# Kernel optimization log

Measured on AMD Instinct MI355X. Metric: run time of the kernel, lower is better.

Reference implementation:

```python
import jax, jax.numpy as jnp
import numpy as np

D_MODEL = 2048
N_Q_HEADS = 32
N_KV_HEADS = 8
D_HEAD = 64
D_MLP = 8192
NORM_EPS = 1e-5
INIT_RANGE = 0.02
IGNORE = -100000.0
B, S = 2, 2048


def setup_inputs() -> dict:
    key = jax.random.key(0)
    ks = jax.random.split(key, 8)
    return {
        "resid_pre": jax.random.normal(ks[0], (B, S, D_MODEL), dtype=jnp.float32),
        "W_Q": jax.random.normal(ks[1], (N_Q_HEADS, D_MODEL, D_HEAD), dtype=jnp.float32) * INIT_RANGE,
        "W_K": jax.random.normal(ks[2], (N_KV_HEADS, D_MODEL, D_HEAD), dtype=jnp.float32) * INIT_RANGE,
        "W_V": jax.random.normal(ks[3], (N_KV_HEADS, D_MODEL, D_HEAD), dtype=jnp.float32) * INIT_RANGE,
        "W_O": jax.random.normal(ks[4], (N_KV_HEADS, D_HEAD, D_MODEL), dtype=jnp.float32) * INIT_RANGE,
        "g1": jnp.ones((D_MODEL,), jnp.float32),
        "b1": jnp.zeros((D_MODEL,), jnp.float32),
        "g2": jnp.ones((D_MODEL,), jnp.float32),
        "b2": jnp.zeros((D_MODEL,), jnp.float32),
        "W_in": jax.random.normal(ks[5], (D_MODEL, D_MLP), dtype=jnp.float32) * INIT_RANGE,
        "b_in": jnp.zeros((D_MLP,), jnp.float32),
        "W_out": jax.random.normal(ks[6], (D_MLP, D_MODEL), dtype=jnp.float32) * INIT_RANGE,
        "b_out": jnp.zeros((D_MODEL,), jnp.float32),
    }


def rmsnorm(x, g, b):
    # torch.var (unbiased=False) is mean-centered variance, but x itself is
    # divided (not centered) -- faithful to the source.
    mu = jnp.mean(x, axis=-1, keepdims=True)
    var = jnp.mean(jnp.square(x - mu), axis=-1, keepdims=True)
    std = jnp.sqrt(var + NORM_EPS)
    return (x / std) * g + b


def attention(x, W_Q, W_K, W_V, W_O):
    b, s, _ = x.shape
    q = jnp.einsum('bpd,hde->bphe', x, W_Q)            # [b, s, n_q, d_head]
    k = jnp.einsum('bpd,hde->bphe', x, W_K)            # [b, s, n_kv, d_head]
    v = jnp.einsum('bpd,hde->bphe', x, W_V)            # [b, s, n_kv, d_head]
    g_size = N_Q_HEADS // N_KV_HEADS
    # rearrange '(n_kv g) d' with n_kv outer, group inner
    q = q.reshape(b, s, N_KV_HEADS, g_size, D_HEAD)
    # source einsum sums over the group dim (g not in output) -- faithful
    scores = jnp.einsum('bqkgd,bskd->bkqs', q, k) / jnp.sqrt(jnp.float32(D_HEAD))
    mask = jnp.triu(jnp.ones((s, s), dtype=bool), k=1)
    scores = jnp.where(mask, jnp.float32(IGNORE), scores)
    pattern = jax.nn.softmax(scores, axis=-1)          # [b, n_kv, q, s]
    z = jnp.einsum('bskd,bkqs->bqkd', v, pattern)      # [b, q, n_kv, d_head]
    return jnp.einsum('bqkd,kde->bqe', z, W_O)


def ffn(x, W_in, b_in, W_out, b_out):
    pre = jnp.einsum('bpd,dm->bpm', x, W_in) + b_in
    post = jax.nn.relu(pre)
    return jnp.einsum('bpm,md->bpd', post, W_out) + b_out


def reference(resid_pre, W_Q, W_K, W_V, W_O, g1, b1, g2, b2, W_in, b_in, W_out, b_out):
    resid_mid = attention(rmsnorm(resid_pre, g1, b1), W_Q, W_K, W_V, W_O) + resid_pre
    resid_post = ffn(rmsnorm(resid_mid, g2, b2), W_in, b_in, W_out, b_out) + resid_mid
    return resid_post
```

## Files before the change

kernel.cpp:

```cpp
#include <hip/hip_runtime.h>
#include <hip/hip_bf16.h>


using bf16 = __hip_bfloat16;
typedef __bf16 bf16x8_t __attribute__((ext_vector_type(8)));
typedef float  f32x4_t  __attribute__((ext_vector_type(4)));

#define D_MODEL 2048
#define SEQ     2048
#define NB      2
#define NTOK    4096
#define NKV     8
#define DHEAD   64
#define DMLP    8192
#define NQKV    1536

__device__ inline void storev(float* p, float v) { *p = v; }
__device__ inline void storev(bf16* p, float v)  { *p = __float2bfloat16(v); }

__device__ inline bf16 h_from_b(__bf16 x) {
    union { __bf16 b; bf16 h; } u;
    u.b = x;
    return u.h;
}

__global__ __launch_bounds__(256) void transpose_f32_bf16_kernel(
    const float* __restrict__ in, bf16* __restrict__ out, int K, int N)
{
    __shared__ float tile[32][33];
    const int n0 = blockIdx.x * 32, k0 = blockIdx.y * 32;
    const int tx = threadIdx.x & 31, ty = threadIdx.x >> 5;
    #pragma unroll
    for (int i = 0; i < 32; i += 8)
        tile[ty + i][tx] = in[(size_t)(k0 + ty + i) * N + n0 + tx];
    __syncthreads();
    #pragma unroll
    for (int i = 0; i < 32; i += 8)
        out[(size_t)(n0 + ty + i) * K + k0 + tx] = __float2bfloat16(tile[tx][ty + i]);
}

__global__ __launch_bounds__(256) void head_transpose_kernel(
    const float* __restrict__ in, bf16* __restrict__ out, int ngroup)
{
    __shared__ float tile[32][65];
    const int kv = blockIdx.y;
    const int k0 = blockIdx.x * 32;
    const int t  = threadIdx.x;
    const int e  = t & 63, kk = t >> 6;
    #pragma unroll
    for (int i = 0; i < 32; i += 4) {
        float s = 0.f;
        for (int g = 0; g < ngroup; ++g)
            s += in[((size_t)(kv * ngroup + g) * 2048 + k0 + kk + i) * 64 + e];
        tile[kk + i][e] = s;
    }
    __syncthreads();
    const int k = t & 31, ee = t >> 5;
    #pragma unroll
    for (int i = 0; i < 64; i += 8)
        out[(size_t)(kv * 64 + ee + i) * 2048 + k0 + k] = __float2bfloat16(tile[k][ee + i]);
}

__global__ __launch_bounds__(256) void rmsnorm_kernel(
    const float* __restrict__ x, const float* __restrict__ g,
    const float* __restrict__ b, bf16* __restrict__ out)
{
    const int row = blockIdx.x;
    const int t = threadIdx.x;
    const float* xr = x + (size_t)row * D_MODEL;
    float4 a0 = *reinterpret_cast<const float4*>(xr + t * 8);
    float4 a1 = *reinterpret_cast<const float4*>(xr + t * 8 + 4);
    float v[8] = {a0.x, a0.y, a0.z, a0.w, a1.x, a1.y, a1.z, a1.w};
    float sum = 0.f, sumsq = 0.f;
    #pragma unroll
    for (int j = 0; j < 8; ++j) { sum += v[j]; sumsq += v[j] * v[j]; }
    #pragma unroll
    for (int o = 1; o < 64; o <<= 1) {
        sum   += __shfl_xor(sum, o);
        sumsq += __shfl_xor(sumsq, o);
    }
    __shared__ float rs[4], rq[4];
    if ((t & 63) == 0) { rs[t >> 6] = sum; rq[t >> 6] = sumsq; }
    __syncthreads();
    sum   = rs[0] + rs[1] + rs[2] + rs[3];
    sumsq = rq[0] + rq[1] + rq[2] + rq[3];
    const float mu  = sum * (1.f / D_MODEL);
    const float var = sumsq * (1.f / D_MODEL) - mu * mu;
    const float rstd = 1.f / sqrtf(var + 1e-5f);
    const int c = t * 8;
    float4 g0 = *reinterpret_cast<const float4*>(g + c);
    float4 g1 = *reinterpret_cast<const float4*>(g + c + 4);
    float4 b0 = *reinterpret_cast<const float4*>(b + c);
    float4 b1 = *reinterpret_cast<const float4*>(b + c + 4);
    float gg[8] = {g0.x, g0.y, g0.z, g0.w, g1.x, g1.y, g1.z, g1.w};
    float bb[8] = {b0.x, b0.y, b0.z, b0.w, b1.x, b1.y, b1.z, b1.w};
    bf16* op = out + (size_t)row * D_MODEL + c;
    #pragma unroll
    for (int j = 0; j < 8; ++j) op[j] = __float2bfloat16(v[j] * rstd * gg[j] + bb[j]);
}

template<int BM, int BN, typename TC, bool BIAS, bool RELU, bool RESID>
__global__ __launch_bounds__(512, 2) void gemm_pipe_kernel(
    const bf16* __restrict__ A, const bf16* __restrict__ Bt,
    TC* __restrict__ C, const float* __restrict__ bias,
    const float* __restrict__ resid, int M, int N, int K, int nbx)
{
    constexpr int BK   = 64;
    constexpr int MREP = BM / 32;
    constexpr int NREP = BN / 64;
    constexpr int AI   = (BM * BK) / 4096;
    constexpr int BI   = (BN * BK) / 4096;
    constexpr int LD   = AI + BI;

    __shared__ __align__(16) bf16 As[2][BM * BK];
    __shared__ __align__(16) bf16 Bs[2][BN * BK];

    const int nwg = gridDim.x;
    const int swz = (blockIdx.x & 7) * (nwg >> 3) + (blockIdx.x >> 3);
    const int nby = nwg / nbx;
    const int by  = swz % nby;
    const int bx  = swz / nby;
    const int row0 = by * BM, col0 = bx * BN;

    const int t  = threadIdx.x;
    const int w  = t >> 6, ln = t & 63;
    const int wm = w >> 2, wn = w & 3;
    const int lr = ln & 15, hi = ln >> 4;

    const int srow = w * 8 + (ln >> 3);
    const int skx  = ((ln & 7) ^ (ln >> 3)) * 8;

    f32x4_t acc[MREP][NREP];
    #pragma unroll
    for (int m = 0; m < MREP; ++m)
        #pragma unroll
        for (int n = 0; n < NREP; ++n) acc[m][n] = (f32x4_t){0.f, 0.f, 0.f, 0.f};

    const int NT = K / BK;

    {
        const bf16* ga = A  + (size_t)(row0 + srow) * K + skx;
        const bf16* gb = Bt + (size_t)(col0 + srow) * K + skx;
        #pragma unroll
        for (int i = 0; i < AI; ++i)
            __builtin_amdgcn_global_load_lds(
                (const __attribute__((address_space(1))) void*)(ga + (size_t)i * 64 * K),
                (__attribute__((address_space(3))) void*)(&As[0][i * 4096 + w * 512]), 16, 0, 0);
        #pragma unroll
        for (int i = 0; i < BI; ++i)
            __builtin_amdgcn_global_load_lds(
                (const __attribute__((address_space(1))) void*)(gb + (size_t)i * 64 * K),
                (__attribute__((address_space(3))) void*)(&Bs[0][i * 4096 + w * 512]), 16, 0, 0);
    }

    for (int tt = 0; tt < NT; ++tt) {
        const int c = tt & 1;
        asm volatile("s_waitcnt lgkmcnt(0)" ::: "memory");
        __builtin_amdgcn_sched_barrier(0);
        __builtin_amdgcn_s_barrier();
        __builtin_amdgcn_sched_barrier(0);
        if (tt + 1 < NT) {
            const int d = c ^ 1;
            const int kt = (tt + 1) * BK;
            const bf16* ga = A  + (size_t)(row0 + srow) * K + kt + skx;
            const bf16* gb = Bt + (size_t)(col0 + srow) * K + kt + skx;
            #pragma unroll
            for (int i = 0; i < AI; ++i)
                __builtin_amdgcn_global_load_lds(
                    (const __attribute__((address_space(1))) void*)(ga + (size_t)i * 64 * K),
                    (__attribute__((address_space(3))) void*)(&As[d][i * 4096 + w * 512]), 16, 0, 0);
            #pragma unroll
            for (int i = 0; i < BI; ++i)
                __builtin_amdgcn_global_load_lds(
                    (const __attribute__((address_space(1))) void*)(gb + (size_t)i * 64 * K),
                    (__attribute__((address_space(3))) void*)(&Bs[d][i * 4096 + w * 512]), 16, 0, 0);
            __builtin_amdgcn_sched_barrier(0);
            if constexpr (LD == 8)      asm volatile("s_waitcnt vmcnt(8)" ::: "memory");
            else if constexpr (LD == 6) asm volatile("s_waitcnt vmcnt(6)" ::: "memory");
            else                        asm volatile("s_waitcnt vmcnt(4)" ::: "memory");
        } else {
            asm volatile("s_waitcnt vmcnt(0)" ::: "memory");
        }
        __builtin_amdgcn_sched_barrier(0);
        __builtin_amdgcn_s_barrier();
        __builtin_amdgcn_sched_barrier(0);

        #pragma unroll
        for (int kk = 0; kk < 2; ++kk) {
            bf16x8_t af[MREP], bfr[NREP];
            #pragma unroll
            for (int m = 0; m < MREP; ++m) {
                const int row = wm * (BM / 2) + m * 16 + lr;
                af[m] = *reinterpret_cast<const bf16x8_t*>(
                    &As[c][row * 64 + ((kk * 32 + hi * 8) ^ ((row & 7) << 3))]);
            }
            #pragma unroll
            for (int n = 0; n < NREP; ++n) {
                const int col = wn * (BN / 4) + n * 16 + lr;
                bfr[n] = *reinterpret_cast<const bf16x8_t*>(
                    &Bs[c][col * 64 + ((kk * 32 + hi * 8) ^ ((col & 7) << 3))]);
            }
            #pragma unroll
            for (int m = 0; m < MREP; ++m)
                #pragma unroll
                for (int n = 0; n < NREP; ++n)
                    acc[m][n] = __builtin_amdgcn_mfma_f32_16x16x32_bf16(af[m], bfr[n], acc[m][n], 0, 0, 0);
        }
    }

    #pragma unroll
    for (int m = 0; m < MREP; ++m) {
        #pragma unroll
        for (int n = 0; n < NREP; ++n) {
            const int cgl = col0 + wn * (BN / 4) + n * 16 + lr;
            #pragma unroll
            for (int j = 0; j < 4; ++j) {
                const int r = row0 + wm * (BM / 2) + m * 16 + hi * 4 + j;
                float v = acc[m][n][j];
                if constexpr (BIAS)  v += bias[cgl];
                if constexpr (RELU)  v = fmaxf(v, 0.f);
                if constexpr (RESID) v += resid[(size_t)r * N + cgl];
                storev(&C[(size_t)r * N + cgl], v);
            }
        }
    }
}

template<typename TC, bool BIAS, bool RELU, bool RESID>
__global__ __launch_bounds__(512, 2) void gemm_8ph_kernel(
    const bf16* __restrict__ A, const bf16* __restrict__ Bt,
    TC* __restrict__ C, const float* __restrict__ bias,
    const float* __restrict__ resid, int M, int N, int K, int nbx)
{
    __shared__ __align__(16) bf16 As[2][256 * 64];
    __shared__ __align__(16) bf16 Bs[2][256 * 64];

    const int nwg = gridDim.x;
    const int swz = (blockIdx.x & 7) * (nwg >> 3) + (blockIdx.x >> 3);
    const int nby = nwg / nbx;
    const int by  = swz % nby;
    const int bx  = swz / nby;
    const int row0 = by * 256, col0 = bx * 256;

    const int t  = threadIdx.x;
    const int w  = t >> 6, ln = t & 63;
    const int wm = w >> 2, wn = w & 3;
    const int lr = ln & 15, hi = ln >> 4;
    const int rx = (lr & 7) << 3;

    const int srow = w * 8 + (ln >> 3);
    const int skx  = ((ln & 7) ^ (ln >> 3)) * 8;

#define STAGE_A8(u, dbuf, kt)                                                   \
    __builtin_amdgcn_global_load_lds(                                           \
        (const __attribute__((address_space(1))) void*)(A + (size_t)(row0 + (u) * 64 + srow) * K + (kt) + skx), \
        (__attribute__((address_space(3))) void*)(&As[dbuf][(u) * 4096 + w * 512]), 16, 0, 0)
#define STAGE_B8(u, dbuf, kt)                                                   \
    __builtin_amdgcn_global_load_lds(                                           \
        (const __attribute__((address_space(1))) void*)(Bt + (size_t)(col0 + (u) * 64 + srow) * K + (kt) + skx), \
        (__attribute__((address_space(3))) void*)(&Bs[dbuf][(u) * 4096 + w * 512]), 16, 0, 0)
#define PH_BAR                                                                  \
    __builtin_amdgcn_sched_barrier(0);                                          \
    __builtin_amdgcn_s_barrier();                                               \
    __builtin_amdgcn_sched_barrier(0)
#define LGKM0                                                                   \
    asm volatile("s_waitcnt lgkmcnt(0)" ::: "memory");                          \
    __builtin_amdgcn_sched_barrier(0)

    f32x4_t acc[8][4];
    #pragma unroll
    for (int m = 0; m < 8; ++m)
        #pragma unroll
        for (int n = 0; n < 4; ++n) acc[m][n] = (f32x4_t){0.f, 0.f, 0.f, 0.f};

    bf16x8_t af[4][2];
    bf16x8_t bfr[4][2];

    const int NT = K / 64;

    STAGE_A8(0, 0, 0); STAGE_A8(2, 0, 0);
    STAGE_B8(0, 0, 0); STAGE_B8(1, 0, 0); STAGE_B8(2, 0, 0); STAGE_B8(3, 0, 0);
    STAGE_A8(1, 0, 0); STAGE_A8(3, 0, 0);
    asm volatile("s_waitcnt vmcnt(2)" ::: "memory");
    PH_BAR;

    for (int tt = 0; tt < NT; ++tt) {
        const int c  = tt & 1, d = c ^ 1;
        const int kn = (tt + 1) * 64;
        const bool pf = (tt + 1 < NT);

        #pragma unroll
        for (int mq = 0; mq < 4; ++mq) {
            const int row = wm * 128 + mq * 16 + lr;
            #pragma unroll
            for (int kk = 0; kk < 2; ++kk)
                af[mq][kk] = *reinterpret_cast<const bf16x8_t*>(
                    &As[c][row * 64 + ((kk * 32 + hi * 8) ^ rx)]);
        }
        #pragma unroll
        for (int n = 0; n < 2; ++n) {
            const int col = wn * 64 + n * 16 + lr;
            #pragma unroll
            for (int kk = 0; kk < 2; ++kk)
                bfr[n][kk] = *reinterpret_cast<const bf16x8_t*>(
                    &Bs[c][col * 64 + ((kk * 32 + hi * 8) ^ rx)]);
        }
        if (pf) { STAGE_A8(0, d, kn); STAGE_A8(2, d, kn); }
        PH_BAR;
        LGKM0;
        __builtin_amdgcn_s_setprio(1);
        #pragma unroll
        for (int mq = 0; mq < 4; ++mq)
            #pragma unroll
            for (int n = 0; n < 2; ++n)
                #pragma unroll
                for (int kk = 0; kk < 2; ++kk)
                    acc[mq][n] = __builtin_amdgcn_mfma_f32_16x16x32_bf16(af[mq][kk], bfr[n][kk], acc[mq][n], 0, 0, 0);
        __builtin_amdgcn_s_setprio(0);
        PH_BAR;

        #pragma unroll
        for (int n = 2; n < 4; ++n) {
            const int col = wn * 64 + n * 16 + lr;
            #pragma unroll
            for (int kk = 0; kk < 2; ++kk)
                bfr[n][kk] = *reinterpret_cast<const bf16x8_t*>(
                    &Bs[c][col * 64 + ((kk * 32 + hi * 8) ^ rx)]);
        }
        if (pf) { STAGE_B8(0, d, kn); STAGE_B8(1, d, kn); }
        __builtin_amdgcn_sched_barrier(0);
        if (pf) { asm volatile("s_waitcnt vmcnt(4)" ::: "memory"); }
        else    { asm volatile("s_waitcnt vmcnt(0)" ::: "memory"); }
        PH_BAR;
        LGKM0;
        __builtin_amdgcn_s_setprio(1);
        #pragma unroll
        for (int mq = 0; mq < 4; ++mq)
            #pragma unroll
            for (int n = 2; n < 4; ++n)
                #pragma unroll
                for (int kk = 0; kk < 2; ++kk)
                    acc[mq][n] = __builtin_amdgcn_mfma_f32_16x16x32_bf16(af[mq][kk], bfr[n][kk], acc[mq][n], 0, 0, 0);
        __builtin_amdgcn_s_setprio(0);
        PH_BAR;

        #pragma unroll
        for (int mq = 0; mq < 4; ++mq) {
            const int row = wm * 128 + 64 + mq * 16 + lr;
            #pragma unroll
            for (int kk = 0; kk < 2; ++kk)
                af[mq][kk] = *reinterpret_cast<const bf16x8_t*>(
                    &As[c][row * 64 + ((kk * 32 + hi * 8) ^ rx)]);
        }
        if (pf) { STAGE_B8(2, d, kn); STAGE_B8(3, d, kn); }
        PH_BAR;
        LGKM0;
        __builtin_amdgcn_s_setprio(1);
        #pragma unroll
        for (int mq = 0; mq < 4; ++mq)
            #pragma unroll
            for (int n = 2; n < 4; ++n)
                #pragma unroll
                for (int kk = 0; kk < 2; ++kk)
                    acc[4 + mq][n] = __builtin_amdgcn_mfma_f32_16x16x32_bf16(af[mq][kk], bfr[n][kk], acc[4 + mq][n], 0, 0, 0);
        __builtin_amdgcn_s_setprio(0);
        PH_BAR;

        if (pf) {
            STAGE_A8(1, d, kn); STAGE_A8(3, d, kn);
            __builtin_amdgcn_sched_barrier(0);
            asm volatile("s_waitcnt vmcnt(2)" ::: "memory");
        }
        PH_BAR;
        __builtin_amdgcn_s_setprio(1);
        #pragma unroll
        for (int mq = 0; mq < 4; ++mq)
            #pragma unroll
            for (int n = 0; n < 2; ++n)
                #pragma unroll
                for (int kk = 0; kk < 2; ++kk)
                    acc[4 + mq][n] = __builtin_amdgcn_mfma_f32_16x16x32_bf16(af[mq][kk], bfr[n][kk], acc[4 + mq][n], 0, 0, 0);
        __builtin_amdgcn_s_setprio(0);
        PH_BAR;
    }

    #pragma unroll
    for (int m = 0; m < 8; ++m) {
        #pragma unroll
        for (int n = 0; n < 4; ++n) {
            const int cgl = col0 + wn * 64 + n * 16 + lr;
            #pragma unroll
            for (int j = 0; j < 4; ++j) {
                const int r = row0 + wm * 128 + m * 16 + hi * 4 + j;
                float v = acc[m][n][j];
                if constexpr (BIAS)  v += bias[cgl];
                if constexpr (RELU)  v = fmaxf(v, 0.f);
                if constexpr (RESID) v += resid[(size_t)r * N + cgl];
                storev(&C[(size_t)r * N + cgl], v);
            }
        }
    }
#undef STAGE_A8
#undef STAGE_B8
#undef PH_BAR
#undef LGKM0
}

#define KVBLK 64
#define LP    72

__global__ __launch_bounds__(256) void mfma_attn_kernel(
    const bf16* __restrict__ qkv, bf16* __restrict__ z)
{
    const int a  = blockIdx.x;
    const int kv = blockIdx.y;
    const int b  = blockIdx.z;
    const int b2 = 31 - a;
    const int t  = threadIdx.x;
    const int w  = t >> 6;
    const int ln = t & 63;
    const int lr = ln & 15;
    const int hi = ln >> 4;
    const int lk = hi * 8;

    __shared__ __align__(16) bf16 Ks[KVBLK * LP];
    __shared__ __align__(16) bf16 Vt[DHEAD * LP];
    __shared__ __align__(16) bf16 Ps[64 * LP];

    bf16x8_t qfA[2], qfB[2];
    #pragma unroll
    for (int sb = 0; sb < 2; ++sb) {
        const int qrow = (sb ? b2 : a) * 64 + w * 16 + lr;
        const bf16* qp = qkv + (size_t)(b * SEQ + qrow) * NQKV + kv * 64;
        #pragma unroll
        for (int kk = 0; kk < 2; ++kk) {
            bf16x8_t v = *reinterpret_cast<const bf16x8_t*>(qp + kk * 32 + lk);
            if (sb) qfB[kk] = v; else qfA[kk] = v;
        }
    }

    f32x4_t accA[4], accB[4];
    #pragma unroll
    for (int n = 0; n < 4; ++n) {
        accA[n] = (f32x4_t){0.f, 0.f, 0.f, 0.f};
        accB[n] = (f32x4_t){0.f, 0.f, 0.f, 0.f};
    }
    float mA[4] = {-1e30f, -1e30f, -1e30f, -1e30f}, lA[4] = {0.f, 0.f, 0.f, 0.f};
    float mB[4] = {-1e30f, -1e30f, -1e30f, -1e30f}, lB[4] = {0.f, 0.f, 0.f, 0.f};

    const int qcdA = a  * 64 + w * 16 + hi * 4;
    const int qcdB = 31 * 64 - a * 64 + w * 16 + hi * 4;

    auto process = [&](const bf16x8_t* qf, f32x4_t* acc_o, float* m_st,
                       float* l_st, int qcd, int k0g, bool diag) {
        f32x4_t s[4];
        #pragma unroll
        for (int n = 0; n < 4; ++n) s[n] = (f32x4_t){0.f, 0.f, 0.f, 0.f};
        #pragma unroll
        for (int kk = 0; kk < 2; ++kk) {
            #pragma unroll
            for (int n = 0; n < 4; ++n) {
                bf16x8_t kf = *reinterpret_cast<const bf16x8_t*>(&Ks[(n * 16 + lr) * LP + kk * 32 + lk]);
                s[n] = __builtin_amdgcn_mfma_f32_16x16x32_bf16(qf[kk], kf, s[n], 0, 0, 0);
            }
        }
        #pragma unroll
        for (int n = 0; n < 4; ++n) {
            const int colg = k0g + n * 16 + lr;
            #pragma unroll
            for (int j = 0; j < 4; ++j) {
                float val = s[n][j] * 0.125f;
                if (diag && colg > qcd + j) val = -1e30f;
                s[n][j] = val;
            }
        }
        float alpha[4], mnew[4];
        #pragma unroll
        for (int j = 0; j < 4; ++j) {
            float mx = fmaxf(fmaxf(s[0][j], s[1][j]), fmaxf(s[2][j], s[3][j]));
            mx = fmaxf(mx, __shfl_xor(mx, 1));
            mx = fmaxf(mx, __shfl_xor(mx, 2));
            mx = fmaxf(mx, __shfl_xor(mx, 4));
            mx = fmaxf(mx, __shfl_xor(mx, 8));
            mnew[j]  = fmaxf(m_st[j], mx);
            alpha[j] = __expf(m_st[j] - mnew[j]);
            m_st[j]  = mnew[j];
        }
        float psum[4] = {0.f, 0.f, 0.f, 0.f};
        #pragma unroll
        for (int n = 0; n < 4; ++n) {
            #pragma unroll
            for (int j = 0; j < 4; ++j) {
                float p = __expf(s[n][j] - mnew[j]);
                psum[j] += p;
                Ps[(w * 16 + hi * 4 + j) * LP + n * 16 + lr] = __float2bfloat16(p);
            }
        }
        #pragma unroll
        for (int j = 0; j < 4; ++j) {
            float ps = psum[j];
            ps += __shfl_xor(ps, 1);
            ps += __shfl_xor(ps, 2);
            ps += __shfl_xor(ps, 4);
            ps += __shfl_xor(ps, 8);
            l_st[j] = l_st[j] * alpha[j] + ps;
        }
        #pragma unroll
        for (int n = 0; n < 4; ++n)
            #pragma unroll
            for (int j = 0; j < 4; ++j)
                acc_o[n][j] *= alpha[j];
        #pragma unroll
        for (int kk = 0; kk < 2; ++kk) {
            bf16x8_t pa = *reinterpret_cast<const bf16x8_t*>(&Ps[(w * 16 + lr) * LP + kk * 32 + lk]);
            #pragma unroll
            for (int n = 0; n < 4; ++n) {
                bf16x8_t vf = *reinterpret_cast<const bf16x8_t*>(&Vt[(n * 16 + lr) * LP + kk * 32 + lk]);
                acc_o[n] = __builtin_amdgcn_mfma_f32_16x16x32_bf16(pa, vf, acc_o[n], 0, 0, 0);
            }
        }
    };

    for (int kt = 0; kt <= b2; ++kt) {
        const int k0g = kt * KVBLK;
        __syncthreads();
        {
            const int r   = t >> 2;
            const int c16 = (t & 3) * 16;
            const bf16* kb = qkv + (size_t)(b * SEQ + k0g + r) * NQKV + 512 + kv * 64 + c16;
            *reinterpret_cast<bf16x8_t*>(&Ks[r * LP + c16])     = *reinterpret_cast<const bf16x8_t*>(kb);
            *reinterpret_cast<bf16x8_t*>(&Ks[r * LP + c16 + 8]) = *reinterpret_cast<const bf16x8_t*>(kb + 8);
        }
        {
            const int dv = w * 16;
            const bf16* vb = qkv + (size_t)(b * SEQ + k0g + ln) * NQKV + 1024 + kv * 64 + dv;
            bf16x8_t v0 = *reinterpret_cast<const bf16x8_t*>(vb);
            bf16x8_t v1 = *reinterpret_cast<const bf16x8_t*>(vb + 8);
            #pragma unroll
            for (int i = 0; i < 8; ++i) {
                Vt[(dv + i)     * LP + ln] = h_from_b(v0[i]);
                Vt[(dv + 8 + i) * LP + ln] = h_from_b(v1[i]);
            }
        }
        __syncthreads();

        if (kt <= a) process(qfA, accA, mA, lA, qcdA, k0g, kt == a);
        process(qfB, accB, mB, lB, qcdB, k0g, kt == b2);
    }

    #pragma unroll
    for (int j = 0; j < 4; ++j) {
        const float invA = 1.f / lA[j];
        bf16* zpA = z + (size_t)(b * SEQ + qcdA + j) * (NKV * DHEAD) + kv * 64;
        const float invB = 1.f / lB[j];
        bf16* zpB = z + (size_t)(b * SEQ + qcdB + j) * (NKV * DHEAD) + kv * 64;
        #pragma unroll
        for (int n = 0; n < 4; ++n) {
            zpA[n * 16 + lr] = __float2bfloat16(accA[n][j] * invA);
            zpB[n * 16 + lr] = __float2bfloat16(accB[n][j] * invB);
        }
    }
}

extern "C" void kernel_launch(void* const* d_in, const int* in_sizes, int n_in,
                              void* d_out, int out_size, void* d_ws, size_t ws_size,
                              hipStream_t stream)
{
    const float* resid_pre = (const float*)d_in[0];
    const float* W_Q   = (const float*)d_in[1];
    const float* W_K   = (const float*)d_in[2];
    const float* W_V   = (const float*)d_in[3];
    const float* W_O   = (const float*)d_in[4];
    const float* g1    = (const float*)d_in[5];
    const float* b1    = (const float*)d_in[6];
    const float* g2    = (const float*)d_in[7];
    const float* b2    = (const float*)d_in[8];
    const float* W_in  = (const float*)d_in[9];
    const float* b_in  = (const float*)d_in[10];
    const float* W_out = (const float*)d_in[11];
    const float* b_out = (const float*)d_in[12];
    float* out = (float*)d_out;

    char* ws = (char*)d_ws;
    const size_t OFF_WBIG  = 0;
    const size_t OFF_WOT   = OFF_WBIG + (size_t)DMLP * D_MODEL * 2;
    const size_t OFF_X1    = OFF_WOT  + (size_t)D_MODEL * 512 * 2;
    const size_t OFF_RMID  = OFF_X1   + (size_t)NTOK * D_MODEL * 2;
    const size_t OFF_POST  = OFF_RMID + (size_t)NTOK * D_MODEL * 4;
    const size_t OFF_WQKVT = OFF_POST;
    const size_t OFF_QKV   = OFF_WQKVT + (size_t)NQKV * D_MODEL * 2;
    const size_t OFF_Z     = OFF_QKV   + (size_t)NTOK * NQKV * 2;

    bf16*  winT   = (bf16*) (ws + OFF_WBIG);
    bf16*  woutT  = (bf16*) (ws + OFF_WBIG);
    bf16*  woT    = (bf16*) (ws + OFF_WOT);
    bf16*  x1     = (bf16*) (ws + OFF_X1);
    float* rmid   = (float*)(ws + OFF_RMID);
    bf16*  post   = (bf16*) (ws + OFF_POST);
    bf16*  wqkvT  = (bf16*) (ws + OFF_WQKVT);
    bf16*  qkv    = (bf16*) (ws + OFF_QKV);
    bf16*  zbuf   = (bf16*) (ws + OFF_Z);

    transpose_f32_bf16_kernel<<<dim3(DMLP / 32, D_MODEL / 32), 256, 0, stream>>>(W_in, winT, D_MODEL, DMLP);
    head_transpose_kernel<<<dim3(D_MODEL / 32, NKV), 256, 0, stream>>>(W_Q, wqkvT, 4);
    head_transpose_kernel<<<dim3(D_MODEL / 32, NKV), 256, 0, stream>>>(W_K, wqkvT + (size_t)512  * D_MODEL, 1);
    head_transpose_kernel<<<dim3(D_MODEL / 32, NKV), 256, 0, stream>>>(W_V, wqkvT + (size_t)1024 * D_MODEL, 1);
    transpose_f32_bf16_kernel<<<dim3(D_MODEL / 32, 512 / 32), 256, 0, stream>>>(W_O, woT, 512, D_MODEL);

    rmsnorm_kernel<<<NTOK, 256, 0, stream>>>(resid_pre, g1, b1, x1);
    gemm_pipe_kernel<128, 128, bf16, false, false, false><<<384, 512, 0, stream>>>(
        x1, wqkvT, qkv, nullptr, nullptr, NTOK, NQKV, D_MODEL, NQKV / 128);
    mfma_attn_kernel<<<dim3(16, NKV, NB), 256, 0, stream>>>(qkv, zbuf);
    gemm_pipe_kernel<128, 128, float, false, false, true><<<512, 512, 0, stream>>>(
        zbuf, woT, rmid, nullptr, resid_pre, NTOK, D_MODEL, 512, D_MODEL / 128);
    rmsnorm_kernel<<<NTOK, 256, 0, stream>>>(rmid, g2, b2, x1);
    gemm_8ph_kernel<bf16, true, true, false><<<512, 512, 0, stream>>>(
        x1, winT, post, b_in, nullptr, NTOK, DMLP, D_MODEL, DMLP / 256);
    transpose_f32_bf16_kernel<<<dim3(D_MODEL / 32, DMLP / 32), 256, 0, stream>>>(W_out, woutT, DMLP, D_MODEL);
    gemm_pipe_kernel<128, 128, float, true, false, true><<<512, 512, 0, stream>>>(
        post, woutT, out, b_out, rmid, NTOK, D_MODEL, DMLP, D_MODEL / 128);
}
```

Measured before the change: 495.2 us.

## Fuse weight transposes into rmsnorm and attention launches to fill idle CUs

Merges the first rmsnorm and the Q/K/V/O weight transposes into one multi-role kernel dispatched by block index. It also folds the W_in transpose into the attention kernel's grid as extra blocks, so the transpose runs alongside the 256 attention blocks. This targets launch overhead and the underfilled GPU during attention. The cost is a larger shared-memory footprint for the transpose blocks and possible contention with attention for memory bandwidth.

```diff
diff --git a/kernel.cpp b/kernel.cpp
--- a/kernel.cpp
+++ b/kernel.cpp
@@ -37,28 +37,6 @@
     #pragma unroll
     for (int i = 0; i < 32; i += 8)
         out[(size_t)(n0 + ty + i) * K + k0 + tx] = __float2bfloat16(tile[tx][ty + i]);
-}
-
-__global__ __launch_bounds__(256) void head_transpose_kernel(
-    const float* __restrict__ in, bf16* __restrict__ out, int ngroup)
-{
-    __shared__ float tile[32][65];
-    const int kv = blockIdx.y;
-    const int k0 = blockIdx.x * 32;
-    const int t  = threadIdx.x;
-    const int e  = t & 63, kk = t >> 6;
-    #pragma unroll
-    for (int i = 0; i < 32; i += 4) {
-        float s = 0.f;
-        for (int g = 0; g < ngroup; ++g)
-            s += in[((size_t)(kv * ngroup + g) * 2048 + k0 + kk + i) * 64 + e];
-        tile[kk + i][e] = s;
-    }
-    __syncthreads();
-    const int k = t & 31, ee = t >> 5;
-    #pragma unroll
-    for (int i = 0; i < 64; i += 8)
-        out[(size_t)(kv * 64 + ee + i) * 2048 + k0 + k] = __float2bfloat16(tile[k][ee + i]);
 }
 
 __global__ __launch_bounds__(256) void rmsnorm_kernel(
@@ -99,6 +77,87 @@
     for (int j = 0; j < 8; ++j) op[j] = __float2bfloat16(v[j] * rstd * gg[j] + bb[j]);
 }
 
+__global__ __launch_bounds__(256) void fusedA_kernel(
+    const float* __restrict__ resid_pre, const float* __restrict__ g1,
+    const float* __restrict__ b1, bf16* __restrict__ x1,
+    const float* __restrict__ WQ, const float* __restrict__ WK,
+    const float* __restrict__ WV, bf16* __restrict__ wqkvT,
+    const float* __restrict__ WO, bf16* __restrict__ woT)
+{
+    __shared__ __align__(16) float smem[32 * 65];
+    const int id = blockIdx.x;
+    const int t  = threadIdx.x;
+
+    if (id < 4096) {
+        float* rs = smem;
+        float* rq = smem + 4;
+        const float* xr = resid_pre + (size_t)id * D_MODEL;
+        float4 a0 = *reinterpret_cast<const float4*>(xr + t * 8);
+        float4 a1 = *reinterpret_cast<const float4*>(xr + t * 8 + 4);
+        float v[8] = {a0.x, a0.y, a0.z, a0.w, a1.x, a1.y, a1.z, a1.w};
+        float sum = 0.f, sumsq = 0.f;
+        #pragma unroll
+        for (int j = 0; j < 8; ++j) { sum += v[j]; sumsq += v[j] * v[j]; }
+        #pragma unroll
+        for (int o = 1; o < 64; o <<= 1) {
+            sum   += __shfl_xor(sum, o);
+            sumsq += __shfl_xor(sumsq, o);
+        }
+        if ((t & 63) == 0) { rs[t >> 6] = sum; rq[t >> 6] = sumsq; }
+        __syncthreads();
+        sum   = rs[0] + rs[1] + rs[2] + rs[3];
+        sumsq = rq[0] + rq[1] + rq[2] + rq[3];
+        const float mu  = sum * (1.f / D_MODEL);
+        const float var = sumsq * (1.f / D_MODEL) - mu * mu;
+        const float rstd = 1.f / sqrtf(var + 1e-5f);
+        const int c = t * 8;
+        float4 g0 = *reinterpret_cast<const float4*>(g1 + c);
+        float4 g1v = *reinterpret_cast<const float4*>(g1 + c + 4);
+        float4 b0 = *reinterpret_cast<const float4*>(b1 + c);
+        float4 b1v = *reinterpret_cast<const float4*>(b1 + c + 4);
+        float gg[8] = {g0.x, g0.y, g0.z, g0.w, g1v.x, g1v.y, g1v.z, g1v.w};
+        float bb[8] = {b0.x, b0.y, b0.z, b0.w, b1v.x, b1v.y, b1v.z, b1v.w};
+        bf16* op = x1 + (size_t)id * D_MODEL + c;
+        #pragma unroll
+        for (int j = 0; j < 8; ++j) op[j] = __float2bfloat16(v[j] * rstd * gg[j] + bb[j]);
+    } else if (id < 5632) {
+        int sub = id - 4096;
+        const int which = sub >> 9;
+        sub &= 511;
+        const float* in = which == 0 ? WQ : (which == 1 ? WK : WV);
+        bf16* outp = wqkvT + (size_t)which * 512 * D_MODEL;
+        const int ngroup = which == 0 ? 4 : 1;
+        const int kv = sub >> 6;
+        const int k0 = (sub & 63) * 32;
+        float (*tile)[65] = reinterpret_cast<float(*)[65]>(smem);
+        const int e  = t & 63, kk = t >> 6;
+        #pragma unroll
+        for (int i = 0; i < 32; i += 4) {
+            float s = 0.f;
+            for (int g = 0; g < ngroup; ++g)
+                s += in[((size_t)(kv * ngroup + g) * 2048 + k0 + kk + i) * 64 + e];
+            tile[kk + i][e] = s;
+        }
+        __syncthreads();
+        const int k = t & 31, ee = t >> 5;
+        #pragma unroll
+        for (int i = 0; i < 64; i += 8)
+            outp[(size_t)(kv * 64 + ee + i) * 2048 + k0 + k] = __float2bfloat16(tile[k][ee + i]);
+    } else {
+        const int sub = id - 5632;
+        const int n0 = (sub & 63) * 32, k0 = (sub >> 6) * 32;
+        float (*tile)[33] = reinterpret_cast<float(*)[33]>(smem);
+        const int tx = t & 31, ty = t >> 5;
+        #pragma unroll
+        for (int i = 0; i < 32; i += 8)
+            tile[ty + i][tx] = WO[(size_t)(k0 + ty + i) * D_MODEL + n0 + tx];
+        __syncthreads();
+        #pragma unroll
+        for (int i = 0; i < 32; i += 8)
+            woT[(size_t)(n0 + ty + i) * 512 + k0 + tx] = __float2bfloat16(tile[tx][ty + i]);
+    }
+}
+
 template<int BM, int BN, typename TC, bool BIAS, bool RELU, bool RESID>
 __global__ __launch_bounds__(512, 2) void gemm_pipe_kernel(
     const bf16* __restrict__ A, const bf16* __restrict__ Bt,
@@ -409,12 +468,30 @@
 #define KVBLK 64
 #define LP    72
 
-__global__ __launch_bounds__(256) void mfma_attn_kernel(
-    const bf16* __restrict__ qkv, bf16* __restrict__ z)
+__global__ __launch_bounds__(256) void fusedB_kernel(
+    const bf16* __restrict__ qkv, bf16* __restrict__ z,
+    const float* __restrict__ W_in, bf16* __restrict__ winT)
 {
-    const int a  = blockIdx.x;
-    const int kv = blockIdx.y;
-    const int b  = blockIdx.z;
+    __shared__ __align__(16) char smem[3 * KVBLK * LP * 2];
+
+    if (blockIdx.x >= 256) {
+        const int sub = blockIdx.x - 256;
+        const int n0 = (sub & 255) * 32, k0 = (sub >> 8) * 32;
+        float (*tile)[33] = reinterpret_cast<float(*)[33]>(smem);
+        const int tx = threadIdx.x & 31, ty = threadIdx.x >> 5;
+        #pragma unroll
+        for (int i = 0; i < 32; i += 8)
+            tile[ty + i][tx] = W_in[(size_t)(k0 + ty + i) * DMLP + n0 + tx];
+        __syncthreads();
+        #pragma unroll
+        for (int i = 0; i < 32; i += 8)
+            winT[(size_t)(n0 + ty + i) * D_MODEL + k0 + tx] = __float2bfloat16(tile[tx][ty + i]);
+        return;
+    }
+
+    const int a  = blockIdx.x & 15;
+    const int kv = (blockIdx.x >> 4) & 7;
+    const int b  = blockIdx.x >> 7;
     const int b2 = 31 - a;
     const int t  = threadIdx.x;
     const int w  = t >> 6;
@@ -423,9 +500,9 @@
     const int hi = ln >> 4;
     const int lk = hi * 8;
 
-    __shared__ __align__(16) bf16 Ks[KVBLK * LP];
-    __shared__ __align__(16) bf16 Vt[DHEAD * LP];
-    __shared__ __align__(16) bf16 Ps[64 * LP];
+    bf16* Ks = reinterpret_cast<bf16*>(smem);
+    bf16* Vt = Ks + KVBLK * LP;
+    bf16* Ps = Vt + DHEAD * LP;
 
     bf16x8_t qfA[2], qfB[2];
     #pragma unroll
@@ -449,7 +526,7 @@
     float mB[4] = {-1e30f, -1e30f, -1e30f, -1e30f}, lB[4] = {0.f, 0.f, 0.f, 0.f};
 
     const int qcdA = a  * 64 + w * 16 + hi * 4;
-    const int qcdB = 31 * 64 - a * 64 + w * 16 + hi * 4;
+    const int qcdB = b2 * 64 + w * 16 + hi * 4;
 
     auto process = [&](const bf16x8_t* qf, f32x4_t* acc_o, float* m_st,
                        float* l_st, int qcd, int k0g, bool diag) {
@@ -601,16 +678,11 @@
     bf16*  qkv    = (bf16*) (ws + OFF_QKV);
     bf16*  zbuf   = (bf16*) (ws + OFF_Z);
 
-    transpose_f32_bf16_kernel<<<dim3(DMLP / 32, D_MODEL / 32), 256, 0, stream>>>(W_in, winT, D_MODEL, DMLP);
-    head_transpose_kernel<<<dim3(D_MODEL / 32, NKV), 256, 0, stream>>>(W_Q, wqkvT, 4);
-    head_transpose_kernel<<<dim3(D_MODEL / 32, NKV), 256, 0, stream>>>(W_K, wqkvT + (size_t)512  * D_MODEL, 1);
-    head_transpose_kernel<<<dim3(D_MODEL / 32, NKV), 256, 0, stream>>>(W_V, wqkvT + (size_t)1024 * D_MODEL, 1);
-    transpose_f32_bf16_kernel<<<dim3(D_MODEL / 32, 512 / 32), 256, 0, stream>>>(W_O, woT, 512, D_MODEL);
-
-    rmsnorm_kernel<<<NTOK, 256, 0, stream>>>(resid_pre, g1, b1, x1);
+    fusedA_kernel<<<4096 + 1536 + 1024, 256, 0, stream>>>(
+        resid_pre, g1, b1, x1, W_Q, W_K, W_V, wqkvT, W_O, woT);
     gemm_pipe_kernel<128, 128, bf16, false, false, false><<<384, 512, 0, stream>>>(
         x1, wqkvT, qkv, nullptr, nullptr, NTOK, NQKV, D_MODEL, NQKV / 128);
-    mfma_attn_kernel<<<dim3(16, NKV, NB), 256, 0, stream>>>(qkv, zbuf);
+    fusedB_kernel<<<256 + 16384, 256, 0, stream>>>(qkv, zbuf, W_in, winT);
     gemm_pipe_kernel<128, 128, float, false, false, true><<<512, 512, 0, stream>>>(
         zbuf, woT, rmid, nullptr, resid_pre, NTOK, D_MODEL, 512, D_MODEL / 128);
     rmsnorm_kernel<<<NTOK, 256, 0, stream>>>(rmid, g2, b2, x1);
```

Measured after the change: 461.1 us. 1.07x faster.
